# Performance work log

Measured on AMD Instinct MI355X. Metric: run time of the kernel, lower is better.

## Reference

```python
import jax, jax.numpy as jnp
import numpy as np

N = 100000
E = 1600000
F_IN = 256
H1, C1 = 8, 8
NUM_CLASSES = 40
NEG_SLOPE = 0.2


def setup_inputs() -> dict:
    key = jax.random.key(0)
    ks = jax.random.split(key, 12)
    x = jax.random.normal(ks[0], (N, F_IN), dtype=jnp.float32)
    ei = jax.random.randint(ks[1], (2, E), 0, N, dtype=jnp.int64)
    # PyG GATConv default add_self_loops=True
    loops = jnp.stack([jnp.arange(N, dtype=jnp.int64)] * 2)
    edge_index = jnp.concatenate([ei, loops], axis=1)  # [2, E+N]
    s1 = 1.0 / np.sqrt(F_IN)
    s2 = 1.0 / np.sqrt(H1 * C1)
    W1 = jax.random.normal(ks[2], (F_IN, H1 * C1), dtype=jnp.float32) * s1
    att_src1 = jax.random.normal(ks[3], (H1, C1), dtype=jnp.float32) * 0.1
    att_dst1 = jax.random.normal(ks[4], (H1, C1), dtype=jnp.float32) * 0.1
    b1 = jnp.zeros((H1 * C1,), dtype=jnp.float32)
    W2 = jax.random.normal(ks[5], (H1 * C1, NUM_CLASSES), dtype=jnp.float32) * s2
    att_src2 = jax.random.normal(ks[6], (1, NUM_CLASSES), dtype=jnp.float32) * 0.1
    att_dst2 = jax.random.normal(ks[7], (1, NUM_CLASSES), dtype=jnp.float32) * 0.1
    b2 = jnp.zeros((NUM_CLASSES,), dtype=jnp.float32)
    return {"x": x, "W1": W1, "att_src1": att_src1, "att_dst1": att_dst1,
            "b1": b1, "W2": W2, "att_src2": att_src2, "att_dst2": att_dst2,
            "b2": b2, "edge_index": edge_index}


def gat_layer(x, W, a_src, a_dst, b, src, dst, heads, out_ch, concat):
    n = x.shape[0]
    h = (x @ W).reshape(n, heads, out_ch)              # [N,H,C]
    alpha_src = (h * a_src[None]).sum(-1)              # [N,H]
    alpha_dst = (h * a_dst[None]).sum(-1)              # [N,H]
    e = jax.nn.leaky_relu(alpha_src[src] + alpha_dst[dst], NEG_SLOPE)  # [E,H]
    m = jax.ops.segment_max(e, dst, num_segments=n)    # per-dst softmax (stable)
    e = jnp.exp(e - m[dst])
    denom = jax.ops.segment_sum(e, dst, num_segments=n)
    w = e / denom[dst]                                 # [E,H]
    msg = h[src] * w[:, :, None]                       # [E,H,C]
    out = jax.ops.segment_sum(msg, dst, num_segments=n)  # [N,H,C]
    out = out.reshape(n, heads * out_ch) if concat else out.mean(axis=1)
    return out + b


def reference(x, W1, att_src1, att_dst1, b1, W2, att_src2, att_dst2, b2, edge_index):
    src, dst = edge_index[0], edge_index[1]
    h = gat_layer(x, W1, att_src1, att_dst1, b1, src, dst, H1, C1, concat=True)
    h = jax.nn.elu(h)
    out = gat_layer(h, W2, att_src2, att_dst2, b2, src, dst, 1, NUM_CLASSES, concat=False)
    return jax.nn.log_softmax(out, axis=1)
```

## Files before the change

### kernel.cpp

```cpp
#include <hip/hip_runtime.h>
#include <hip/hip_bf16.h>

#define NEG_SLOPE 0.2f

typedef __attribute__((ext_vector_type(8))) short short8;
typedef __attribute__((ext_vector_type(4))) float f32x4;

__device__ __forceinline__ float lrelu(float x) { return x >= 0.f ? x : NEG_SLOPE * x; }

__device__ __forceinline__ unsigned pack_bf2(float a, float b) {
    unsigned ua = __float_as_uint(a), ub = __float_as_uint(b);
    ua = (ua + 0x7fffu + ((ua >> 16) & 1u)) >> 16;
    ub = (ub + 0x7fffu + ((ub >> 16) & 1u)) & 0xffff0000u;
    return ua | ub;
}
__device__ __forceinline__ float2 unpack_bf2(unsigned u) {
    return make_float2(__uint_as_float(u << 16), __uint_as_float(u & 0xffff0000u));
}
__device__ __forceinline__ unsigned short bf16_of(float a) {
    unsigned ua = __float_as_uint(a);
    return (unsigned short)((ua + 0x7fffu + ((ua >> 16) & 1u)) >> 16);
}

__global__ __launch_bounds__(256) void bcount_kernel(const int* __restrict__ dst,
                                                     int* __restrict__ blk_cnt,
                                                     int etot, int psz, int chunk) {
    __shared__ int cnt[8];
    if (threadIdx.x < 8) cnt[threadIdx.x] = 0;
    __syncthreads();
    int e0 = blockIdx.x * chunk, e1 = min(etot, e0 + chunk);
    for (int e = e0 + (int)threadIdx.x; e < e1; e += 256) {
        int p = min(dst[e] / psz, 7);
        atomicAdd(&cnt[p], 1);
    }
    __syncthreads();
    if (threadIdx.x < 8) blk_cnt[blockIdx.x * 8 + threadIdx.x] = cnt[threadIdx.x];
}

__global__ __launch_bounds__(1024) void bscan_kernel(const int* __restrict__ blk_cnt,
                                                     int* __restrict__ blk_base,
                                                     int* __restrict__ bstart) {
    __shared__ int wsum[16];
    __shared__ int coltot[8];
    __shared__ int colbase[9];
    int t = threadIdx.x;
    int lane = t & 63, wid = t >> 6;
    int v[8], incl[8];
#pragma unroll
    for (int p = 0; p < 8; ++p) v[p] = blk_cnt[t * 8 + p];
#pragma unroll
    for (int p = 0; p < 8; ++p) {
        int x = v[p];
#pragma unroll
        for (int off = 1; off < 64; off <<= 1) {
            int y = __shfl_up(x, off);
            if (lane >= off) x += y;
        }
        if (lane == 63) wsum[wid] = x;
        __syncthreads();
        if (wid == 0) {
            int s = (lane < 16) ? wsum[lane] : 0;
#pragma unroll
            for (int off = 1; off < 16; off <<= 1) {
                int y = __shfl_up(s, off);
                if (lane >= off) s += y;
            }
            if (lane < 16) wsum[lane] = s;
        }
        __syncthreads();
        int base = (wid > 0) ? wsum[wid - 1] : 0;
        incl[p] = base + x;
        if (t == 1023) coltot[p] = incl[p];
        __syncthreads();
    }
    if (t == 0) {
        int acc = 0;
        for (int p = 0; p < 8; ++p) {
            colbase[p] = acc;
            bstart[p] = acc;
            acc += coltot[p];
        }
        colbase[8] = acc;
        bstart[8] = acc;
    }
    __syncthreads();
#pragma unroll
    for (int p = 0; p < 8; ++p) blk_base[t * 8 + p] = colbase[p] + incl[p] - v[p];
}

__global__ __launch_bounds__(256) void bscatter_kernel(const int* __restrict__ src,
                                                       const int* __restrict__ dst,
                                                       const int* __restrict__ blk_base,
                                                       int* __restrict__ src_b,
                                                       int* __restrict__ dst_b,
                                                       int etot, int psz, int chunk) {
    __shared__ int base[8];
    __shared__ int lcnt[8];
    if (threadIdx.x < 8) {
        base[threadIdx.x] = blk_base[blockIdx.x * 8 + threadIdx.x];
        lcnt[threadIdx.x] = 0;
    }
    __syncthreads();
    int e0 = blockIdx.x * chunk, e1 = min(etot, e0 + chunk);
    for (int e = e0 + (int)threadIdx.x; e < e1; e += 256) {
        int d = dst[e], s = src[e];
        int p = min(d / psz, 7);
        int loc = atomicAdd(&lcnt[p], 1);
        int pos = base[p] + loc;
        dst_b[pos] = d;
        src_b[pos] = s;
    }
}

__global__ __launch_bounds__(256) void histB_kernel(const int* __restrict__ dst_b,
                                                    const int* __restrict__ bstart,
                                                    int* __restrict__ counts,
                                                    int* __restrict__ pk) {
    int part = blockIdx.x & 7, stripe = blockIdx.x >> 3;
    int nstripes = gridDim.x >> 3;
    int b0 = bstart[part], b1 = bstart[part + 1];
    int per = (b1 - b0 + nstripes - 1) / nstripes;
    int e0 = b0 + stripe * per, e1 = min(b1, e0 + per);
    for (int e = e0 + (int)threadIdx.x; e < e1; e += 256) {
        int d = dst_b[e];
        int r = atomicAdd(&counts[d], 1);
        pk[e] = d | (r << 17);
    }
}

__global__ __launch_bounds__(256) void scanA_kernel(const int* __restrict__ counts,
                                                    int* __restrict__ bsums, int n) {
    __shared__ int sm[256];
    int i = blockIdx.x * 256 + threadIdx.x;
    sm[threadIdx.x] = (i < n) ? counts[i] : 0;
    __syncthreads();
    for (int off = 128; off > 0; off >>= 1) {
        if (threadIdx.x < off) sm[threadIdx.x] += sm[threadIdx.x + off];
        __syncthreads();
    }
    if (threadIdx.x == 0) bsums[blockIdx.x] = sm[0];
}

__global__ __launch_bounds__(1024) void scanB_kernel(int* __restrict__ bsums, int nb) {
    __shared__ int sm[1024];
    int t = threadIdx.x;
    int v = (t < nb) ? bsums[t] : 0;
    sm[t] = v;
    __syncthreads();
    for (int off = 1; off < 1024; off <<= 1) {
        int u = (t >= off) ? sm[t - off] : 0;
        __syncthreads();
        sm[t] += u;
        __syncthreads();
    }
    if (t < nb) bsums[t] = sm[t] - v;
}

__global__ __launch_bounds__(256) void scanC_kernel(const int* __restrict__ counts,
                                                    const int* __restrict__ bsums,
                                                    int* __restrict__ row_ptr, int n, int etot) {
    __shared__ int sm[256];
    int t = threadIdx.x;
    int i = blockIdx.x * 256 + t;
    int v = (i < n) ? counts[i] : 0;
    sm[t] = v;
    __syncthreads();
    for (int off = 1; off < 256; off <<= 1) {
        int u = (t >= off) ? sm[t - off] : 0;
        __syncthreads();
        sm[t] += u;
        __syncthreads();
    }
    if (i < n) row_ptr[i] = bsums[blockIdx.x] + sm[t] - v;
    if (i == 0) row_ptr[n] = etot;
}

__global__ __launch_bounds__(256) void scatterB_kernel(const int* __restrict__ src_b,
                                                       const int* __restrict__ pk,
                                                       const int* __restrict__ bstart,
                                                       const int* __restrict__ row_ptr,
                                                       int* __restrict__ csr_src) {
    int part = blockIdx.x & 7, stripe = blockIdx.x >> 3;
    int nstripes = gridDim.x >> 3;
    int b0 = bstart[part], b1 = bstart[part + 1];
    int per = (b1 - b0 + nstripes - 1) / nstripes;
    int e0 = b0 + stripe * per, e1 = min(b1, e0 + per);
    for (int e = e0 + (int)threadIdx.x; e < e1; e += 256) {
        unsigned v = (unsigned)pk[e];
        int d = (int)(v & 131071u);
        int r = (int)(v >> 17);
        csr_src[row_ptr[d] + r] = src_b[e];
    }
}

__global__ __launch_bounds__(256) void w1cvt_kernel(const float* __restrict__ W1,
                                                    unsigned short* __restrict__ W1t) {
    int t = blockIdx.x * 256 + threadIdx.x;
    int k = t >> 6, nn = t & 63;
    W1t[(size_t)nn * 256 + k] = bf16_of(W1[t]);
}

__global__ __launch_bounds__(256) void gemm1_kernel(const float* __restrict__ x,
                                                    const unsigned short* __restrict__ W1t,
                                                    unsigned short* __restrict__ h1b, int n) {
    int tid = threadIdx.x;
    int w = tid >> 6, lane = tid & 63;
    int p = lane & 15, quad = lane >> 4;
    int r0 = blockIdx.x * 64;
    int row = r0 + 16 * w + p;
    const float* xrow = x + (size_t)row * 256;
    f32x4 z = {0.f, 0.f, 0.f, 0.f};
    f32x4 acc[4] = {z, z, z, z};
#pragma unroll
    for (int kc = 0; kc < 8; ++kc) {
        int k0 = kc * 32 + quad * 8;
        float4 v0 = make_float4(0.f, 0.f, 0.f, 0.f), v1 = v0;
        if (row < n) {
            v0 = *(const float4*)(xrow + k0);
            v1 = *(const float4*)(xrow + k0 + 4);
        }
        union { uint4 u; short8 s; } a;
        a.u = make_uint4(pack_bf2(v0.x, v0.y), pack_bf2(v0.z, v0.w),
                         pack_bf2(v1.x, v1.y), pack_bf2(v1.z, v1.w));
#pragma unroll
        for (int t = 0; t < 4; ++t) {
            short8 b = *(const short8*)(W1t + (size_t)(16 * t + p) * 256 + k0);
            acc[t] = __builtin_amdgcn_mfma_f32_16x16x32_bf16(a.s, b, acc[t], 0, 0, 0);
        }
    }
#pragma unroll
    for (int t = 0; t < 4; ++t)
#pragma unroll
        for (int r = 0; r < 4; ++r) {
            int gr = r0 + 16 * w + quad * 4 + r;
            if (gr < n) h1b[(size_t)gr * 64 + 16 * t + p] = bf16_of(acc[t][r]);
        }
}

__global__ __launch_bounds__(256) void alpha1_kernel(const unsigned short* __restrict__ h1b,
                                                     const float* __restrict__ att_s,
                                                     const float* __restrict__ att_d,
                                                     float* __restrict__ as1,
                                                     float* __restrict__ ad1, int n) {
    int wid = threadIdx.x >> 6, lane = threadIdx.x & 63;
    int p = lane & 31;
    int r = blockIdx.x * 8 + wid * 2 + (lane >> 5);
    if (r >= n) return;
    float2 sc = *(const float2*)(att_s + 2 * p);
    float2 dc = *(const float2*)(att_d + 2 * p);
    float2 h = unpack_bf2(((const unsigned*)h1b)[(size_t)r * 32 + p]);
    float ps = h.x * sc.x + h.y * sc.y;
    float pd = h.x * dc.x + h.y * dc.y;
    ps += __shfl_xor(ps, 1); pd += __shfl_xor(pd, 1);
    ps += __shfl_xor(ps, 2); pd += __shfl_xor(pd, 2);
    if ((p & 3) == 0) {
        as1[(size_t)r * 8 + (p >> 2)] = ps;
        ad1[(size_t)r * 8 + (p >> 2)] = pd;
    }
}

__global__ __launch_bounds__(256) void agg1_kernel(const unsigned short* __restrict__ h1b,
                                                   const float* __restrict__ as1,
                                                   const float* __restrict__ ad1,
                                                   const float* __restrict__ b1,
                                                   const int* __restrict__ row_ptr,
                                                   const int* __restrict__ csr_src,
                                                   float* __restrict__ elu1, int n) {
    int lane = threadIdx.x & 63;
    int node = blockIdx.x * 4 + (threadIdx.x >> 6);
    if (node >= n) return;
    int start = row_ptr[node], end = row_ptr[node + 1];
    int slot = lane >> 3, hd = lane & 7;
    float adh = ad1[(size_t)node * 8 + hd];

    float m = -1e30f, den = 0.f;
    for (int base = start; base < end; base += 64) {
        int nloc = min(64, end - base);
        int eidx = base + lane;
        int sAll = (eidx < end) ? csr_src[eidx] : 0;
        for (int e0 = 0; e0 < nloc; e0 += 16) {
            int s0 = __shfl(sAll, e0 + slot);
            int s1 = __shfl(sAll, e0 + 8 + slot);
            float v0 = lrelu(as1[(size_t)s0 * 8 + hd] + adh);
            float v1 = lrelu(as1[(size_t)s1 * 8 + hd] + adh);
            if (e0 + slot >= nloc) v0 = -INFINITY;
            if (e0 + 8 + slot >= nloc) v1 = -INFINITY;
            float nm = fmaxf(m, fmaxf(v0, v1));
            den = den * __expf(m - nm) + __expf(v0 - nm) + __expf(v1 - nm);
            m = nm;
        }
    }
#pragma unroll
    for (int off = 8; off < 64; off <<= 1) {
        float om = __shfl_xor(m, off);
        float od = __shfl_xor(den, off);
        float nm = fmaxf(m, om);
        den = den * __expf(m - nm) + od * __expf(om - nm);
        m = nm;
    }
    float inv = 1.f / den;

    int q = lane >> 5, p = lane & 31, hp = p >> 2;
    const unsigned* h1u = (const unsigned*)h1b;
    float2 o = make_float2(0.f, 0.f);
    for (int base = start; base < end; base += 64) {
        int nloc = min(64, end - base);
        int eidx = base + lane;
        int sAll = (eidx < end) ? csr_src[eidx] : 0;
        for (int e0 = 0; e0 < nloc; e0 += 8) {
            int s = __shfl(sAll, e0 + slot);
            float v = lrelu(as1[(size_t)s * 8 + hd] + adh);
            float w = (e0 + slot < nloc) ? __expf(v - m) * inv : 0.f;
#pragma unroll
            for (int j = 0; j < 8; j += 2) {
                int sj = __shfl(s, (j + q) * 8);
                float wj = __shfl(w, (j + q) * 8 + hp);
                float2 hf = unpack_bf2(h1u[(size_t)sj * 32 + p]);
                o.x = fmaf(hf.x, wj, o.x);
                o.y = fmaf(hf.y, wj, o.y);
            }
        }
    }
    o.x += __shfl_xor(o.x, 32);
    o.y += __shfl_xor(o.y, 32);
    if (lane < 32) {
        float2 bb = *(const float2*)(b1 + 2 * p);
        float v0 = o.x + bb.x, v1 = o.y + bb.y;
        v0 = v0 > 0.f ? v0 : __expf(v0) - 1.f;
        v1 = v1 > 0.f ? v1 : __expf(v1) - 1.f;
        *(float2*)(elu1 + (size_t)node * 64 + 2 * p) = make_float2(v0, v1);
    }
}

__global__ __launch_bounds__(256) void gemm2_kernel(const float* __restrict__ elu1,
                                                    const float* __restrict__ W2,
                                                    const float* __restrict__ att_s,
                                                    const float* __restrict__ att_d,
                                                    unsigned short* __restrict__ h2b,
                                                    float* __restrict__ as2,
                                                    float* __restrict__ ad2, int n) {
    __shared__ float As[64][132];
    __shared__ float Bs[64][40];
    int tid = threadIdx.x;
    int r0 = blockIdx.x * 128;
    int cx = tid & 7, ry = tid >> 3;
    float sa[5], da[5];
#pragma unroll
    for (int j = 0; j < 5; ++j) {
        sa[j] = att_s[5 * cx + j];
        da[j] = att_d[5 * cx + j];
    }
    for (int t = tid; t < 640; t += 256) {
        int k = t / 10, cq = t % 10;
        *(float4*)&Bs[k][4 * cq] = *(const float4*)(W2 + (size_t)k * 40 + 4 * cq);
    }
    for (int t = tid; t < 2048; t += 256) {
        int row = t >> 4, kq = t & 15;
        int gr = r0 + row;
        float4 av = make_float4(0.f, 0.f, 0.f, 0.f);
        if (gr < n) av = *(const float4*)(elu1 + (size_t)gr * 64 + 4 * kq);
        As[4 * kq + 0][row] = av.x;
        As[4 * kq + 1][row] = av.y;
        As[4 * kq + 2][row] = av.z;
        As[4 * kq + 3][row] = av.w;
    }
    __syncthreads();
    float acc[4][5] = {{0.f}};
#pragma unroll 8
    for (int k = 0; k < 64; ++k) {
        float4 a = *(const float4*)&As[k][4 * ry];
        float ar[4] = {a.x, a.y, a.z, a.w};
        float br[5];
#pragma unroll
        for (int j = 0; j < 5; ++j) br[j] = Bs[k][5 * cx + j];
#pragma unroll
        for (int i = 0; i < 4; ++i)
#pragma unroll
            for (int j = 0; j < 5; ++j) acc[i][j] = fmaf(ar[i], br[j], acc[i][j]);
    }
#pragma unroll
    for (int i = 0; i < 4; ++i) {
        int gr = r0 + 4 * ry + i;
        float ps = 0.f, pd = 0.f;
#pragma unroll
        for (int j = 0; j < 5; ++j) {
            ps = fmaf(acc[i][j], sa[j], ps);
            pd = fmaf(acc[i][j], da[j], pd);
        }
        ps += __shfl_xor(ps, 1); pd += __shfl_xor(pd, 1);
        ps += __shfl_xor(ps, 2); pd += __shfl_xor(pd, 2);
        ps += __shfl_xor(ps, 4); pd += __shfl_xor(pd, 4);
        if (gr < n) {
#pragma unroll
            for (int j = 0; j < 5; ++j) h2b[(size_t)gr * 40 + 5 * cx + j] = bf16_of(acc[i][j]);
            if (cx == 0) {
                as2[gr] = ps;
                ad2[gr] = pd;
            }
        }
    }
}

__global__ __launch_bounds__(256) void agg2_kernel(const unsigned short* __restrict__ h2b,
                                                   const float* __restrict__ as2,
                                                   const float* __restrict__ ad2,
                                                   const float* __restrict__ b2,
                                                   const int* __restrict__ row_ptr,
                                                   const int* __restrict__ csr_src,
                                                   float* __restrict__ out, int n) {
    int lane = threadIdx.x & 63;
    int node = blockIdx.x * 4 + (threadIdx.x >> 6);
    if (node >= n) return;
    int start = row_ptr[node], end = row_ptr[node + 1];
    float adn = ad2[node];

    float m = -1e30f, den = 0.f;
    for (int base = start; base < end; base += 64) {
        int eidx = base + lane;
        bool valid = eidx < end;
        int s = valid ? csr_src[eidx] : 0;
        float v = lrelu(as2[s] + adn);
        if (!valid) v = -INFINITY;
        float nm = fmaxf(m, v);
        den = den * __expf(m - nm) + __expf(v - nm);
        m = nm;
    }
#pragma unroll
    for (int off = 1; off < 64; off <<= 1) {
        float om = __shfl_xor(m, off);
        float od = __shfl_xor(den, off);
        float nm = fmaxf(m, om);
        den = den * __expf(m - nm) + od * __expf(om - nm);
        m = nm;
    }
    float inv = 1.f / den;

    int q = lane >> 5, p = lane & 31;
    int pc = min(p, 19);
    const unsigned* h2u = (const unsigned*)h2b;
    float2 o = make_float2(0.f, 0.f);
    for (int base = start; base < end; base += 64) {
        int nloc = min(64, end - base);
        int eidx = base + lane;
        bool valid = eidx < end;
        int sAll = valid ? csr_src[eidx] : 0;
        float v = lrelu(as2[sAll] + adn);
        float w = valid ? __expf(v - m) * inv : 0.f;
        for (int g = 0; g < nloc; g += 8) {
#pragma unroll
            for (int j = 0; j < 8; j += 2) {
                int idx = g + j + q;
                int sj = __shfl(sAll, idx);
                float wj = __shfl(w, idx);
                float2 hf = unpack_bf2(h2u[(size_t)sj * 20 + pc]);
                o.x = fmaf(hf.x, wj, o.x);
                o.y = fmaf(hf.y, wj, o.y);
            }
        }
    }
    o.x += __shfl_xor(o.x, 32);
    o.y += __shfl_xor(o.y, 32);
    bool act = (lane < 32) && (p < 20);
    float v0 = -1e30f, v1 = -1e30f;
    if (act) {
        float2 bb = *(const float2*)(b2 + 2 * p);
        v0 = o.x + bb.x;
        v1 = o.y + bb.y;
    }
    float vm = fmaxf(v0, v1);
#pragma unroll
    for (int off = 1; off < 64; off <<= 1) vm = fmaxf(vm, __shfl_xor(vm, off));
    float ex = act ? (__expf(v0 - vm) + __expf(v1 - vm)) : 0.f;
#pragma unroll
    for (int off = 1; off < 64; off <<= 1) ex += __shfl_xor(ex, off);
    if (act) {
        float lg = __logf(ex);
        *(float2*)(out + (size_t)node * 40 + 2 * p) = make_float2(v0 - vm - lg, v1 - vm - lg);
    }
}

extern "C" void kernel_launch(void* const* d_in, const int* in_sizes, int n_in,
                              void* d_out, int out_size, void* d_ws, size_t ws_size,
                              hipStream_t stream) {
    const float* x        = (const float*)d_in[0];
    const float* W1       = (const float*)d_in[1];
    const float* att_src1 = (const float*)d_in[2];
    const float* att_dst1 = (const float*)d_in[3];
    const float* b1       = (const float*)d_in[4];
    const float* W2       = (const float*)d_in[5];
    const float* att_src2 = (const float*)d_in[6];
    const float* att_dst2 = (const float*)d_in[7];
    const float* b2       = (const float*)d_in[8];
    const int*   ei       = (const int*)d_in[9];

    int n    = in_sizes[0] / 256;
    int etot = in_sizes[9] / 2;
    const int* srcp = ei;
    const int* dstp = ei + etot;

    char* ws = (char*)d_ws;
    size_t off = 0;
    unsigned short* h1b = (unsigned short*)(ws + off); off += (size_t)n * 64 * 2;
    unsigned short* h2b = (unsigned short*)(ws + off); off += (size_t)n * 40 * 2;
    unsigned short* W1t = (unsigned short*)(ws + off); off += (size_t)64 * 256 * 2;
    float* elu1 = (float*)(ws + off); off += (size_t)n * 64 * 4;
    float* as1  = (float*)(ws + off); off += (size_t)n * 8 * 4;
    float* ad1  = (float*)(ws + off); off += (size_t)n * 8 * 4;
    float* as2  = (float*)(ws + off); off += (size_t)n * 4;
    float* ad2  = (float*)(ws + off); off += (size_t)n * 4;
    int* row_ptr = (int*)(ws + off); off += (size_t)(n + 64) * 4;
    int* counts  = (int*)(ws + off); off += (size_t)n * 4;
    int* bsums   = (int*)(ws + off); off += (size_t)2048 * 4;
    int* csr_src = (int*)(ws + off); off += (size_t)etot * 4;
    int* blk_cnt = (int*)(ws + off); off += (size_t)1024 * 8 * 4;
    int* blk_base= (int*)(ws + off); off += (size_t)1024 * 8 * 4;
    int* bstart  = (int*)(ws + off); off += (size_t)16 * 4;
    float* outp = (float*)d_out;

    int* src_b = (int*)elu1;
    int* dst_b = src_b + etot;
    int* pk    = dst_b + etot;

    int psz = (n + 7) >> 3;
    int chunk = (etot + 1023) / 1024;

    hipMemsetAsync(counts, 0, (size_t)n * 4, stream);
    int nb256 = (n + 255) / 256;
    bcount_kernel<<<1024, 256, 0, stream>>>(dstp, blk_cnt, etot, psz, chunk);
    bscan_kernel<<<1, 1024, 0, stream>>>(blk_cnt, blk_base, bstart);
    bscatter_kernel<<<1024, 256, 0, stream>>>(srcp, dstp, blk_base, src_b, dst_b, etot, psz, chunk);
    histB_kernel<<<2048, 256, 0, stream>>>(dst_b, bstart, counts, pk);
    scanA_kernel<<<nb256, 256, 0, stream>>>(counts, bsums, n);
    scanB_kernel<<<1, 1024, 0, stream>>>(bsums, nb256);
    scanC_kernel<<<nb256, 256, 0, stream>>>(counts, bsums, row_ptr, n, etot);
    scatterB_kernel<<<2048, 256, 0, stream>>>(src_b, pk, bstart, row_ptr, csr_src);

    int nb4 = (n + 3) / 4;
    w1cvt_kernel<<<64, 256, 0, stream>>>(W1, W1t);
    gemm1_kernel<<<(n + 63) / 64, 256, 0, stream>>>(x, W1t, h1b, n);
    alpha1_kernel<<<(n + 7) / 8, 256, 0, stream>>>(h1b, att_src1, att_dst1, as1, ad1, n);
    agg1_kernel<<<nb4, 256, 0, stream>>>(h1b, as1, ad1, b1, row_ptr, csr_src, elu1, n);
    gemm2_kernel<<<(n + 127) / 128, 256, 0, stream>>>(elu1, W2, att_src2, att_dst2, h2b, as2, ad2, n);
    agg2_kernel<<<nb4, 256, 0, stream>>>(h2b, as2, ad2, b2, row_ptr, csr_src, outp, n);
}
```

Before: 459.5 us.

## Fuse softmax normalization into aggregation pass, dropping max-subtraction pre-pass

Both aggregation kernels previously made a separate pass over each node's edges to compute the running max and the softmax denominator, then a second pass to gather features. The new code makes a single pass: it accumulates unnormalized exp(logit) weights and their sum together, then divides the aggregated features by the sum at the end. This removes one full pass of csr_src reads and attention-score gathers per node. The trade-off is that the stabilizing max subtraction is gone, so large attention logits could overflow exp. That is safe only while logits stay small, as they do with these input scales.

```diff
diff --git a/kernel.cpp b/kernel.cpp
--- a/kernel.cpp
+++ b/kernel.cpp
@@ -272,37 +272,10 @@
     int start = row_ptr[node], end = row_ptr[node + 1];
     int slot = lane >> 3, hd = lane & 7;
     float adh = ad1[(size_t)node * 8 + hd];
-
-    float m = -1e30f, den = 0.f;
-    for (int base = start; base < end; base += 64) {
-        int nloc = min(64, end - base);
-        int eidx = base + lane;
-        int sAll = (eidx < end) ? csr_src[eidx] : 0;
-        for (int e0 = 0; e0 < nloc; e0 += 16) {
-            int s0 = __shfl(sAll, e0 + slot);
-            int s1 = __shfl(sAll, e0 + 8 + slot);
-            float v0 = lrelu(as1[(size_t)s0 * 8 + hd] + adh);
-            float v1 = lrelu(as1[(size_t)s1 * 8 + hd] + adh);
-            if (e0 + slot >= nloc) v0 = -INFINITY;
-            if (e0 + 8 + slot >= nloc) v1 = -INFINITY;
-            float nm = fmaxf(m, fmaxf(v0, v1));
-            den = den * __expf(m - nm) + __expf(v0 - nm) + __expf(v1 - nm);
-            m = nm;
-        }
-    }
-#pragma unroll
-    for (int off = 8; off < 64; off <<= 1) {
-        float om = __shfl_xor(m, off);
-        float od = __shfl_xor(den, off);
-        float nm = fmaxf(m, om);
-        den = den * __expf(m - nm) + od * __expf(om - nm);
-        m = nm;
-    }
-    float inv = 1.f / den;
-
     int q = lane >> 5, p = lane & 31, hp = p >> 2;
     const unsigned* h1u = (const unsigned*)h1b;
     float2 o = make_float2(0.f, 0.f);
+    float den = 0.f;
     for (int base = start; base < end; base += 64) {
         int nloc = min(64, end - base);
         int eidx = base + lane;
@@ -310,7 +283,8 @@
         for (int e0 = 0; e0 < nloc; e0 += 8) {
             int s = __shfl(sAll, e0 + slot);
             float v = lrelu(as1[(size_t)s * 8 + hd] + adh);
-            float w = (e0 + slot < nloc) ? __expf(v - m) * inv : 0.f;
+            float w = (e0 + slot < nloc) ? __expf(v) : 0.f;
+            den += w;
 #pragma unroll
             for (int j = 0; j < 8; j += 2) {
                 int sj = __shfl(s, (j + q) * 8);
@@ -321,11 +295,15 @@
             }
         }
     }
+    den += __shfl_xor(den, 8);
+    den += __shfl_xor(den, 16);
+    den += __shfl_xor(den, 32);
+    float inv = 1.f / __shfl(den, hp);
     o.x += __shfl_xor(o.x, 32);
     o.y += __shfl_xor(o.y, 32);
     if (lane < 32) {
         float2 bb = *(const float2*)(b1 + 2 * p);
-        float v0 = o.x + bb.x, v1 = o.y + bb.y;
+        float v0 = o.x * inv + bb.x, v1 = o.y * inv + bb.y;
         v0 = v0 > 0.f ? v0 : __expf(v0) - 1.f;
         v1 = v1 > 0.f ? v1 : __expf(v1) - 1.f;
         *(float2*)(elu1 + (size_t)node * 64 + 2 * p) = make_float2(v0, v1);
@@ -414,38 +392,19 @@
     int start = row_ptr[node], end = row_ptr[node + 1];
     float adn = ad2[node];
 
-    float m = -1e30f, den = 0.f;
-    for (int base = start; base < end; base += 64) {
-        int eidx = base + lane;
-        bool valid = eidx < end;
-        int s = valid ? csr_src[eidx] : 0;
-        float v = lrelu(as2[s] + adn);
-        if (!valid) v = -INFINITY;
-        float nm = fmaxf(m, v);
-        den = den * __expf(m - nm) + __expf(v - nm);
-        m = nm;
-    }
-#pragma unroll
-    for (int off = 1; off < 64; off <<= 1) {
-        float om = __shfl_xor(m, off);
-        float od = __shfl_xor(den, off);
-        float nm = fmaxf(m, om);
-        den = den * __expf(m - nm) + od * __expf(om - nm);
-        m = nm;
-    }
-    float inv = 1.f / den;
-
     int q = lane >> 5, p = lane & 31;
     int pc = min(p, 19);
     const unsigned* h2u = (const unsigned*)h2b;
     float2 o = make_float2(0.f, 0.f);
+    float den = 0.f;
     for (int base = start; base < end; base += 64) {
         int nloc = min(64, end - base);
         int eidx = base + lane;
         bool valid = eidx < end;
         int sAll = valid ? csr_src[eidx] : 0;
         float v = lrelu(as2[sAll] + adn);
-        float w = valid ? __expf(v - m) * inv : 0.f;
+        float w = valid ? __expf(v) : 0.f;
+        den += w;
         for (int g = 0; g < nloc; g += 8) {
 #pragma unroll
             for (int j = 0; j < 8; j += 2) {
@@ -458,14 +417,17 @@
             }
         }
     }
+#pragma unroll
+    for (int off = 1; off < 64; off <<= 1) den += __shfl_xor(den, off);
+    float inv = 1.f / den;
     o.x += __shfl_xor(o.x, 32);
     o.y += __shfl_xor(o.y, 32);
     bool act = (lane < 32) && (p < 20);
     float v0 = -1e30f, v1 = -1e30f;
     if (act) {
         float2 bb = *(const float2*)(b2 + 2 * p);
-        v0 = o.x + bb.x;
-        v1 = o.y + bb.y;
+        v0 = o.x * inv + bb.x;
+        v1 = o.y * inv + bb.y;
     }
     float vm = fmaxf(v0, v1);
 #pragma unroll
```

Measured after the change: 439.0 us. 1.05x faster.
